# Optimization experiments

Hardware: AMD Instinct MI355X
Metric: run time of the kernel (lower is better)

The kernel has to match this reference:

```python
import jax, jax.numpy as jnp
import numpy as np

ATTN_MASK_VALUE = -1e10
N = 8192
DIM = 1024
DIM_HEAD = 64
DIM_OUT = 1024

def setup_inputs() -> dict:
    key = jax.random.key(0)
    k1, k2, k3 = jax.random.split(key, 3)
    x = jax.random.normal(k1, (N, DIM), dtype=jnp.float32)
    Wqkv = jax.random.normal(k2, (DIM, 3 * DIM_HEAD), dtype=jnp.float32) * (DIM ** -0.5)
    Wout = jax.random.normal(k3, (DIM_HEAD, DIM_OUT), dtype=jnp.float32) * (DIM_HEAD ** -0.5)
    bout = jnp.zeros((DIM_OUT,), dtype=jnp.float32)
    return {"x": x, "Wqkv": Wqkv, "Wout": Wout, "bout": bout}

def reference(x, Wqkv, Wout, bout) -> jnp.ndarray:
    n = x.shape[0]
    scale = DIM_HEAD ** -0.5
    qkv = x @ Wqkv                      # [n, 3*dh]
    q, k, v = jnp.split(qkv, 3, axis=-1)  # each [n, dh]
    sim = jnp.einsum('id,jd->ij', q, k) * scale  # [n, n]
    mask = jnp.tril(jnp.ones((n, n), dtype=bool))
    sim = jnp.where(mask, sim, ATTN_MASK_VALUE)
    attn = jax.nn.softmax(sim, axis=-1)
    out = jnp.einsum('ij,jd->id', attn, v)  # [n, dh]
    return out @ Wout + bout            # [n, dim_out]
```

## Files before the change

### kernel.cpp

```cpp
#include <hip/hip_runtime.h>
#include <hip/hip_bf16.h>

#define N_TOK 8192
#define RREC 4352

typedef float f32x4  __attribute__((ext_vector_type(4)));
typedef float f32x16 __attribute__((ext_vector_type(16)));
typedef short bf16x8 __attribute__((ext_vector_type(8)));
typedef unsigned int u32x4 __attribute__((ext_vector_type(4)));

__device__ inline short f2bf(float f) {
    union { __hip_bfloat16 h; short s; } u;
    u.h = __float2bfloat16(f);
    return u.s;
}
__device__ inline unsigned cvtpk(float lo, float hi) {
    unsigned r;
    asm("v_cvt_pk_bf16_f32 %0, %1, %2" : "=v"(r) : "v"(lo), "v"(hi));
    return r;
}
__device__ inline void plswap(unsigned &a, unsigned &b) {
    asm("v_permlane32_swap_b32 %0, %1" : "+v"(a), "+v"(b));
}
__device__ inline void gload_lds16(const __hip_bfloat16* g, __hip_bfloat16* s) {
    __builtin_amdgcn_global_load_lds(
        (const __attribute__((address_space(1))) void*)(g),
        (__attribute__((address_space(3))) void*)(s), 16, 0, 0);
}


__global__ __launch_bounds__(256) void conv_kernel(
    const float* __restrict__ Wqkv,
    const float* __restrict__ Wout,
    __hip_bfloat16* __restrict__ Wt,
    __hip_bfloat16* __restrict__ WoT) {
    __shared__ float tile[32][33];
    const int t = threadIdx.x;
    const int cc = t & 31, rbase = t >> 5;
    const int b = blockIdx.x;
    if (b < 192) {
        const int r0 = (b & 31) * 32;
        const int c0 = (b >> 5) * 32;
        #pragma unroll
        for (int it = 0; it < 4; ++it) {
            const int rr = rbase + it * 8;
            tile[rr][cc] = Wqkv[(size_t)(r0 + rr) * 192 + c0 + cc];
        }
        __syncthreads();
        #pragma unroll
        for (int it = 0; it < 4; ++it) {
            const int rr = rbase + it * 8;
            Wt[(size_t)(c0 + rr) * 1024 + r0 + cc] = __float2bfloat16(tile[cc][rr]);
        }
    } else {
        const int bb = b - 192;
        const int r0 = (bb & 1) * 32;
        const int c0 = (bb >> 1) * 32;
        #pragma unroll
        for (int it = 0; it < 4; ++it) {
            const int rr = rbase + it * 8;
            tile[rr][cc] = Wout[(size_t)(r0 + rr) * 1024 + c0 + cc];
        }
        __syncthreads();
        #pragma unroll
        for (int it = 0; it < 4; ++it) {
            const int rr = rbase + it * 8;
            WoT[(size_t)(c0 + rr) * 64 + r0 + cc] = __float2bfloat16(tile[cc][rr]);
        }
    }
}

__global__ __launch_bounds__(256) void qkv_kernel(
    const float* __restrict__ x,
    const __hip_bfloat16* __restrict__ Wt,
    __hip_bfloat16* __restrict__ Qf,
    __hip_bfloat16* __restrict__ Kf,
    __hip_bfloat16* __restrict__ Vf) {
    __shared__ __hip_bfloat16 sA[2][16 * 64];
    __shared__ __hip_bfloat16 sB[2][192 * 64];
    __shared__ __hip_bfloat16 sV[64][20];
    const int tid = threadIdx.x;
    const int w = tid >> 6, lane = tid & 63;
    const int l16 = lane & 15, lq = lane >> 4;
    const int m0 = blockIdx.x * 16;

    const int ar = tid >> 4;
    const int ac = (tid & 15) >> 1;
    const int ah = tid & 1;
    const float* agp = x + (size_t)(m0 + ar) * 1024 + ac * 8 + ah * 4;
    const int aoff = ar * 64 + ((ac ^ (ar & 7)) * 8) + ah * 4;

    int boff[6];
    const __hip_bfloat16* bgp[6];
    #pragma unroll
    for (int i = 0; i < 6; ++i) {
        const int q = i * 256 + tid;
        const int r = q >> 3, c = q & 7;
        bgp[i] = Wt + (size_t)r * 1024 + c * 8;
        boff[i] = r * 64 + ((c ^ (r & 7)) * 8);
    }

    const int arow = l16;
    const int aswz0 = arow * 64 + ((lq ^ (arow & 7)) * 8);
    const int aswz1 = arow * 64 + (((4 + lq) ^ (arow & 7)) * 8);
    int bswz0[3], bswz1[3];
    #pragma unroll
    for (int j = 0; j < 3; ++j) {
        const int row = (w * 3 + j) * 16 + l16;
        bswz0[j] = row * 64 + ((lq ^ (row & 7)) * 8);
        bswz1[j] = row * 64 + (((4 + lq) ^ (row & 7)) * 8);
    }

    f32x4 acc[3];
    #pragma unroll
    for (int j = 0; j < 3; ++j) acc[j] = (f32x4)0.f;

    float4 areg;
    u32x4 breg[6];

    areg = *reinterpret_cast<const float4*>(agp);
    #pragma unroll
    for (int i = 0; i < 6; ++i)
        breg[i] = *reinterpret_cast<const u32x4*>(bgp[i]);
    {
        uint2 aw; aw.x = cvtpk(areg.x, areg.y); aw.y = cvtpk(areg.z, areg.w);
        *reinterpret_cast<uint2*>(&sA[0][aoff]) = aw;
        #pragma unroll
        for (int i = 0; i < 6; ++i)
            *reinterpret_cast<u32x4*>(&sB[0][boff[i]]) = breg[i];
    }
    __syncthreads();

    for (int ks = 0; ks < 16; ++ks) {
        const int cur = ks & 1;
        if (ks < 15) {
            areg = *reinterpret_cast<const float4*>(agp + (ks + 1) * 64);
            #pragma unroll
            for (int i = 0; i < 6; ++i)
                breg[i] = *reinterpret_cast<const u32x4*>(bgp[i] + (ks + 1) * 64);
        }
        bf16x8 af0 = *reinterpret_cast<const bf16x8*>(&sA[cur][aswz0]);
        bf16x8 af1 = *reinterpret_cast<const bf16x8*>(&sA[cur][aswz1]);
        #pragma unroll
        for (int j = 0; j < 3; ++j) {
            bf16x8 b0 = *reinterpret_cast<const bf16x8*>(&sB[cur][bswz0[j]]);
            bf16x8 b1 = *reinterpret_cast<const bf16x8*>(&sB[cur][bswz1[j]]);
            acc[j] = __builtin_amdgcn_mfma_f32_16x16x32_bf16(b0, af0, acc[j], 0, 0, 0);
            acc[j] = __builtin_amdgcn_mfma_f32_16x16x32_bf16(b1, af1, acc[j], 0, 0, 0);
        }
        if (ks < 15) {
            uint2 aw; aw.x = cvtpk(areg.x, areg.y); aw.y = cvtpk(areg.z, areg.w);
            *reinterpret_cast<uint2*>(&sA[cur ^ 1][aoff]) = aw;
            #pragma unroll
            for (int i = 0; i < 6; ++i)
                *reinterpret_cast<u32x4*>(&sB[cur ^ 1][boff[i]]) = breg[i];
        }
        __syncthreads();
    }

    const int row = m0 + l16;
    #pragma unroll
    for (int j = 0; j < 3; ++j) {
        const int nt = w * 3 + j;
        const int nb = nt * 16 + 4 * lq;
        if (nt < 4) {
            const int tq = row >> 5, lr = row & 31;
            const int kc = nb >> 4, hi2 = (nb >> 3) & 1, jj = nb & 7;
            short4 qs;
            qs.x = f2bf(acc[j][0] * 0.18033688011112042f);
            qs.y = f2bf(acc[j][1] * 0.18033688011112042f);
            qs.z = f2bf(acc[j][2] * 0.18033688011112042f);
            qs.w = f2bf(acc[j][3] * 0.18033688011112042f);
            *reinterpret_cast<short4*>(Qf + ((size_t)(tq * 4 + kc) * 64 + lr + 32 * hi2) * 8 + jj) = qs;
        } else if (nt < 8) {
            const int col = nb - 64;
            const int c = row >> 6, rr = row & 63, hk = rr >> 5, lr = rr & 31;
            const int kc = col >> 4, hi2 = (col >> 3) & 1, jj = col & 7;
            short4 ks4;
            ks4.x = f2bf(acc[j][0]); ks4.y = f2bf(acc[j][1]);
            ks4.z = f2bf(acc[j][2]); ks4.w = f2bf(acc[j][3]);
            *reinterpret_cast<short4*>(Kf + ((size_t)(c * 8 + 4 * hk + kc) * 64 + lr + 32 * hi2) * 8 + jj) = ks4;
        } else {
            #pragma unroll
            for (int r = 0; r < 4; ++r)
                sV[nb + r - 128][l16] = __float2bfloat16(acc[j][r]);
        }
    }
    __syncthreads();
    const int vd = tid >> 2, vm = (tid & 3) * 4;
    short4 vv = *reinterpret_cast<const short4*>(&sV[vd][vm]);
    const int kv = m0 + vm;
    const int c = kv >> 6, ks2 = (kv >> 4) & 3, hi2 = (kv >> 3) & 1, jj = kv & 7;
    *reinterpret_cast<short4*>(Vf + ((size_t)(c * 8 + 4 * (vd >> 5) + ks2) * 64 + (vd & 31) + 32 * hi2) * 8 + jj) = vv;
}

__global__ __launch_bounds__(512, 4) void attn_kernel(
    const __hip_bfloat16* __restrict__ Qf,
    const __hip_bfloat16* __restrict__ Kf,
    const __hip_bfloat16* __restrict__ Vf,
    char* __restrict__ Part) {
    __shared__ __hip_bfloat16 sK[2][4096];
    __shared__ __hip_bfloat16 sV2[2][4096];
    const int tid = threadIdx.x;
    const int w = tid >> 6, lane = tid & 63;
    const int l31 = lane & 31, hi = lane >> 5;
    const int bid = blockIdx.x;
    const int qb = (bid < 256) ? (63 - (bid >> 3)) : ((bid - 256) >> 3);
    const int s = bid & 7;
    const int tsub = w >> 1, h = w & 1;
    const int tq = qb * 4 + tsub;
    const int q0 = tq * 32;
    const int qabs = q0 + l31;
    const int CtB = 2 * qb + 2;
    const int nst = (CtB > s) ? ((CtB - s + 7) >> 3) : 0;

    bf16x8 qf[4];
    #pragma unroll
    for (int kc = 0; kc < 4; ++kc)
        qf[kc] = *reinterpret_cast<const bf16x8*>(
            Qf + ((size_t)(tq * 4 + kc) * 64 + lane) * 8);

    float l = 0.f;
    f32x16 Oa = (f32x16)0.f, Oc = (f32x16)0.f;

    const size_t gofs = (size_t)w * 512 + lane * 8;

    if (nst > 0) gload_lds16(Kf + (size_t)s * 4096 + gofs, &sK[0][w * 512]),
                 gload_lds16(Vf + (size_t)s * 4096 + gofs, &sV2[0][w * 512]);
    __syncthreads();

    int cur = 0;
    for (int st = 0; st < nst; ++st) {
        const int c = s + st * 8;
        if (st + 1 < nst) {
            gload_lds16(Kf + (size_t)(c + 8) * 4096 + gofs, &sK[cur ^ 1][w * 512]);
            gload_lds16(Vf + (size_t)(c + 8) * 4096 + gofs, &sV2[cur ^ 1][w * 512]);
        }

        const int kv0h = c * 64 + h * 32;
        if (kv0h <= q0 + 31) {
            f32x16 Sa = (f32x16)(-16.f);
            #pragma unroll
            for (int kc = 0; kc < 4; ++kc) {
                bf16x8 ka = *reinterpret_cast<const bf16x8*>(
                    &sK[cur][((4 * h + kc) * 64 + lane) * 8]);
                Sa = __builtin_amdgcn_mfma_f32_32x32x16_bf16(ka, qf[kc], Sa, 0, 0, 0);
            }

            if (kv0h + 32 > q0) {
                #pragma unroll
                for (int r = 0; r < 16; ++r) {
                    const int rowk = (r & 3) + 8 * (r >> 2) + 4 * hi;
                    if (kv0h + rowk > qabs) Sa[r] = -1.0e30f;
                }
            }

            #pragma unroll
            for (int r = 0; r < 16; ++r) Sa[r] = exp2f(Sa[r]);
            float s8[8];
            #pragma unroll
            for (int j = 0; j < 8; ++j) s8[j] = Sa[2 * j] + Sa[2 * j + 1];
            #pragma unroll
            for (int j = 0; j < 4; ++j) s8[j] += s8[j + 4];
            float ps = (s8[0] + s8[2]) + (s8[1] + s8[3]);
            ps += __shfl_xor(ps, 32);
            l += ps;

            bf16x8 F0, F1;
            {
                unsigned a0 = cvtpk(Sa[0], Sa[1]),  a1 = cvtpk(Sa[2], Sa[3]);
                unsigned a2 = cvtpk(Sa[4], Sa[5]),  a3 = cvtpk(Sa[6], Sa[7]);
                plswap(a0, a2); plswap(a1, a3);
                u32x4 w0; w0[0] = a0; w0[1] = a1; w0[2] = a2; w0[3] = a3;
                F0 = __builtin_bit_cast(bf16x8, w0);
                unsigned b0 = cvtpk(Sa[8], Sa[9]),  b1 = cvtpk(Sa[10], Sa[11]);
                unsigned b2 = cvtpk(Sa[12], Sa[13]), b3 = cvtpk(Sa[14], Sa[15]);
                plswap(b0, b2); plswap(b1, b3);
                u32x4 w1; w1[0] = b0; w1[1] = b1; w1[2] = b2; w1[3] = b3;
                F1 = __builtin_bit_cast(bf16x8, w1);
            }
            #pragma unroll
            for (int ks = 0; ks < 2; ++ks) {
                bf16x8 Fk = ks ? F1 : F0;
                bf16x8 v0 = *reinterpret_cast<const bf16x8*>(
                    &sV2[cur][((2 * h + ks) * 64 + lane) * 8]);
                bf16x8 v1 = *reinterpret_cast<const bf16x8*>(
                    &sV2[cur][((4 + 2 * h + ks) * 64 + lane) * 8]);
                Oa = __builtin_amdgcn_mfma_f32_32x32x16_bf16(v0, Fk, Oa, 0, 0, 0);
                Oc = __builtin_amdgcn_mfma_f32_32x32x16_bf16(v1, Fk, Oc, 0, 0, 0);
            }
        }

        __syncthreads();
        cur ^= 1;
    }

    char* rec = Part + ((size_t)tq * 16 + s * 2 + h) * RREC;
    __hip_bfloat16* On = (__hip_bfloat16*)rec;
    const float invl = (l > 0.f) ? (1.0f / l) : 0.f;
    #pragma unroll
    for (int r = 0; r < 16; ++r) {
        const int d = (r & 3) + 8 * (r >> 2) + 4 * hi;
        On[d * 32 + l31]        = __float2bfloat16(Oa[r] * invl);
        On[(d + 32) * 32 + l31] = __float2bfloat16(Oc[r] * invl);
    }
    if (hi == 0) ((float*)(rec + 4096))[l31] = l;
}

__global__ __launch_bounds__(256) void mo_kernel(
    const char* __restrict__ Part,
    const __hip_bfloat16* __restrict__ WoT,
    const float* __restrict__ bout,
    float* __restrict__ out) {
    __shared__ __hip_bfloat16 sOb[32][72];
    const int tid = threadIdx.x;
    const int t = blockIdx.x, q0 = t * 32;
    const char* base = Part + (size_t)t * 16 * RREC;

    for (int e = tid; e < 2048; e += 256) {
        const int qq = e & 31, d = e >> 5;
        float ll = 0.f, oo = 0.f;
        #pragma unroll
        for (int rid = 0; rid < 16; ++rid) {
            const char* rec = base + rid * RREC;
            const float ls = ((const float*)(rec + 4096))[qq];
            ll += ls;
            oo += ls * __bfloat162float(((const __hip_bfloat16*)rec)[d * 32 + qq]);
        }
        sOb[qq][d] = __float2bfloat16(oo / ll);
    }
    __syncthreads();

    const int w = tid >> 6, lane = tid & 63;
    const int l16 = lane & 15, lq = lane >> 4;
    const int colq = w * 256;

    for (int nt = 0; nt < 16; ++nt) {
        const int cb = colq + nt * 16;
        const __hip_bfloat16* wrow = WoT + (size_t)(cb + l16) * 64;
        bf16x8 b0 = *reinterpret_cast<const bf16x8*>(wrow + 8 * lq);
        bf16x8 b1 = *reinterpret_cast<const bf16x8*>(wrow + 32 + 8 * lq);
        const int nb = cb + 4 * lq;
        float4 bb = *reinterpret_cast<const float4*>(bout + nb);
        #pragma unroll
        for (int rt = 0; rt < 2; ++rt) {
            const int arow = rt * 16 + l16;
            bf16x8 a0 = *reinterpret_cast<const bf16x8*>(&sOb[arow][8 * lq]);
            bf16x8 a1 = *reinterpret_cast<const bf16x8*>(&sOb[arow][32 + 8 * lq]);
            f32x4 acc = (f32x4)0.f;
            acc = __builtin_amdgcn_mfma_f32_16x16x32_bf16(b0, a0, acc, 0, 0, 0);
            acc = __builtin_amdgcn_mfma_f32_16x16x32_bf16(b1, a1, acc, 0, 0, 0);
            const int row = q0 + rt * 16 + l16;
            float4 res;
            res.x = acc[0] + bb.x; res.y = acc[1] + bb.y;
            res.z = acc[2] + bb.z; res.w = acc[3] + bb.w;
            *reinterpret_cast<float4*>(out + (size_t)row * 1024 + nb) = res;
        }
    }
}

extern "C" void kernel_launch(void* const* d_in, const int* in_sizes, int n_in,
                              void* d_out, int out_size, void* d_ws, size_t ws_size,
                              hipStream_t stream) {
    const float* x    = (const float*)d_in[0];
    const float* Wqkv = (const float*)d_in[1];
    const float* Wout = (const float*)d_in[2];
    const float* bout = (const float*)d_in[3];
    float* out = (float*)d_out;

    char* ws = (char*)d_ws;
    __hip_bfloat16* Wt  = (__hip_bfloat16*)(ws);
    __hip_bfloat16* WoT = (__hip_bfloat16*)(ws + 393216);
    __hip_bfloat16* Qf  = (__hip_bfloat16*)(ws + 524288);
    __hip_bfloat16* Kf  = (__hip_bfloat16*)(ws + 1572864);
    __hip_bfloat16* Vf  = (__hip_bfloat16*)(ws + 2621440);
    char*           Part = ws + 4718592;

    conv_kernel<<<256, 256, 0, stream>>>(Wqkv, Wout, Wt, WoT);
    qkv_kernel<<<512, 256, 0, stream>>>(x, Wt, Qf, Kf, Vf);
    attn_kernel<<<512, 512, 0, stream>>>(Qf, Kf, Vf, Part);
    mo_kernel<<<256, 256, 0, stream>>>(Part, WoT, bout, out);
}
```

Measured before the change: 66.11 us.

## Merge the two per-block half partials in LDS before writing global records

Result: no change. 65.35 us (-1.1%).

```diff
diff --git a/kernel.cpp b/kernel.cpp
--- a/kernel.cpp
+++ b/kernel.cpp
@@ -295,16 +295,32 @@
         cur ^= 1;
     }
 
-    char* rec = Part + ((size_t)tq * 16 + s * 2 + h) * RREC;
-    __hip_bfloat16* On = (__hip_bfloat16*)rec;
-    const float invl = (l > 0.f) ? (1.0f / l) : 0.f;
-    #pragma unroll
-    for (int r = 0; r < 16; ++r) {
-        const int d = (r & 3) + 8 * (r >> 2) + 4 * hi;
-        On[d * 32 + l31]        = __float2bfloat16(Oa[r] * invl);
-        On[(d + 32) * 32 + l31] = __float2bfloat16(Oc[r] * invl);
-    }
-    if (hi == 0) ((float*)(rec + 4096))[l31] = l;
+    __hip_bfloat16* exO = (__hip_bfloat16*)sK;
+    float* exL = (float*)sV2;
+    if (h == 1) {
+        #pragma unroll
+        for (int r = 0; r < 16; ++r) {
+            const int d = (r & 3) + 8 * (r >> 2) + 4 * hi;
+            exO[tsub * 2048 + d * 32 + l31]        = __float2bfloat16(Oa[r]);
+            exO[tsub * 2048 + (d + 32) * 32 + l31] = __float2bfloat16(Oc[r]);
+        }
+        if (hi == 0) exL[tsub * 32 + l31] = l;
+    }
+    __syncthreads();
+    if (h == 0) {
+        char* rec = Part + ((size_t)tq * 8 + s) * RREC;
+        __hip_bfloat16* On = (__hip_bfloat16*)rec;
+        #pragma unroll
+        for (int r = 0; r < 16; ++r) {
+            const int d = (r & 3) + 8 * (r >> 2) + 4 * hi;
+            On[d * 32 + l31] = __float2bfloat16(
+                Oa[r] + __bfloat162float(exO[tsub * 2048 + d * 32 + l31]));
+            On[(d + 32) * 32 + l31] = __float2bfloat16(
+                Oc[r] + __bfloat162float(exO[tsub * 2048 + (d + 32) * 32 + l31]));
+        }
+        if (hi == 0)
+            ((float*)(rec + 4096))[l31] = l + exL[tsub * 32 + l31];
+    }
 }
 
 __global__ __launch_bounds__(256) void mo_kernel(
@@ -315,17 +331,16 @@
     __shared__ __hip_bfloat16 sOb[32][72];
     const int tid = threadIdx.x;
     const int t = blockIdx.x, q0 = t * 32;
-    const char* base = Part + (size_t)t * 16 * RREC;
+    const char* base = Part + (size_t)t * 8 * RREC;
 
     for (int e = tid; e < 2048; e += 256) {
         const int qq = e & 31, d = e >> 5;
         float ll = 0.f, oo = 0.f;
         #pragma unroll
-        for (int rid = 0; rid < 16; ++rid) {
+        for (int rid = 0; rid < 8; ++rid) {
             const char* rec = base + rid * RREC;
-            const float ls = ((const float*)(rec + 4096))[qq];
-            ll += ls;
-            oo += ls * __bfloat162float(((const __hip_bfloat16*)rec)[d * 32 + qq]);
+            ll += ((const float*)(rec + 4096))[qq];
+            oo += __bfloat162float(((const __hip_bfloat16*)rec)[d * 32 + qq]);
         }
         sOb[qq][d] = __float2bfloat16(oo / ll);
     }
```
